# Kernel tuning notes

Hardware: AMD Instinct MI355X
Metric: run time of the kernel (lower is better)

The kernel has to match this reference:

```python
import math
import jax, jax.numpy as jnp
import numpy as np

D_MODEL = 1024
NUM_HEADS = 16
HEAD_DIM = D_MODEL // NUM_HEADS
BATCH = 4
SEQ = 2048


def setup_inputs() -> dict:
    key = jax.random.key(0)
    ks = jax.random.split(key, 9)
    scale = 1.0 / math.sqrt(D_MODEL)
    return {
        "x": jax.random.normal(ks[0], (BATCH, SEQ, D_MODEL), dtype=jnp.float32),
        "wq": jax.random.normal(ks[1], (D_MODEL, D_MODEL), dtype=jnp.float32) * scale,
        "bq": jnp.zeros((D_MODEL,), dtype=jnp.float32),
        "wk": jax.random.normal(ks[2], (D_MODEL, D_MODEL), dtype=jnp.float32) * scale,
        "bk": jnp.zeros((D_MODEL,), dtype=jnp.float32),
        "wv": jax.random.normal(ks[3], (D_MODEL, D_MODEL), dtype=jnp.float32) * scale,
        "bv": jnp.zeros((D_MODEL,), dtype=jnp.float32),
        "wo": jax.random.normal(ks[4], (D_MODEL, D_MODEL), dtype=jnp.float32) * scale,
        "bo": jnp.zeros((D_MODEL,), dtype=jnp.float32),
    }


def _split_heads(t):
    b, s, _ = t.shape
    return t.reshape(b, s, NUM_HEADS, HEAD_DIM).transpose(0, 2, 1, 3)  # [b,h,s,d]


def reference(x, wq, bq, wk, bk, wv, bv, wo, bo):
    # Linear layers: y = x @ W^T + b (torch nn.Linear convention)
    q = _split_heads(x @ wq.T + bq)
    k = _split_heads(x @ wk.T + bk)
    v = _split_heads(x @ wv.T + bv)
    scores = jnp.einsum("bhqd,bhkd->bhqk", q, k) / math.sqrt(HEAD_DIM)
    attn_weights = jax.nn.softmax(scores, axis=-1)  # dropout=0.0 (eval) -> identity
    context = jnp.einsum("bhqk,bhkd->bhqd", attn_weights, v)
    context = context.transpose(0, 2, 1, 3).reshape(x.shape[0], x.shape[1], D_MODEL)
    output = context @ wo.T + bo
    return output, attn_weights
```

## Files before the change

kernel.cpp:

```cpp
#include <hip/hip_runtime.h>
#include <cstdint>
#include <cstddef>


#define D_MODEL 1024
#define NHEADS  16
#define HDIM    64
#define BATCH   4
#define SEQ     2048
#define NTOK    (BATCH*SEQ)

typedef __bf16 bf16x8 __attribute__((ext_vector_type(8)));
typedef float  f32x4  __attribute__((ext_vector_type(4)));
typedef unsigned short u16x8 __attribute__((ext_vector_type(8)));

__device__ __forceinline__ uint16_t f2bf(float f) {
  union { float f; uint32_t u; } v; v.f = f;
  return (uint16_t)((v.u + 0x7FFFu + ((v.u >> 16) & 1u)) >> 16);
}
__device__ __forceinline__ float bf2f(uint16_t u) {
  union { uint32_t u; float f; } v; v.u = (uint32_t)u << 16; return v.f;
}
__device__ __forceinline__ bf16x8 ldbf8(const uint16_t* p) {
  return __builtin_bit_cast(bf16x8, *(const u16x8*)p);
}
__device__ __forceinline__ void nt_store4(float* p, float a, float b, float c, float d) {
  f32x4 v = { a, b, c, d };
  __builtin_nontemporal_store(v, (f32x4*)p);
}
#define MFMA16(a, b, c) __builtin_amdgcn_mfma_f32_16x16x32_bf16((a), (b), (c), 0, 0, 0)

__device__ __forceinline__ void gl_lds16(const uint16_t* g, uint16_t* l) {
  __builtin_amdgcn_global_load_lds(
      (const __attribute__((address_space(1))) uint32_t*)g,
      (__attribute__((address_space(3))) uint32_t*)l, 16, 0, 0);
}

__global__ __launch_bounds__(256) void cvt_kernel(const float* __restrict__ src,
                                                  uint16_t* __restrict__ dst, int n4) {
  int i = blockIdx.x * blockDim.x + threadIdx.x;
  if (i < n4) {
    float4 f = ((const float4*)src)[i];
    ushort4 o;
    o.x = f2bf(f.x); o.y = f2bf(f.y); o.z = f2bf(f.z); o.w = f2bf(f.w);
    ((ushort4*)dst)[i] = o;
  }
}
__global__ __launch_bounds__(256)
void cvt_w_kernel(const float* __restrict__ wq, const float* __restrict__ wk,
                  const float* __restrict__ wv, const float* __restrict__ wo,
                  uint16_t* __restrict__ dst) {
  int i = blockIdx.x * blockDim.x + threadIdx.x;
  int sel = i >> 18, off = i & 262143;
  const float* src = (sel == 0) ? wq : (sel == 1) ? wk : (sel == 2) ? wv : wo;
  float4 f = ((const float4*)src)[off];
  ushort4 o;
  o.x = f2bf(f.x); o.y = f2bf(f.y); o.z = f2bf(f.z); o.w = f2bf(f.w);
  ((ushort4*)dst)[i] = o;
}

__global__ __launch_bounds__(256)
void gemm_qkv(const uint16_t* __restrict__ A, const uint16_t* __restrict__ Wqkv,
              const float* __restrict__ bq, const float* __restrict__ bk,
              const float* __restrict__ bv,
              uint16_t* __restrict__ Qb, uint16_t* __restrict__ Kc,
              uint16_t* __restrict__ Vt) {
  __shared__ uint16_t As[128 * 64];
  __shared__ uint16_t Bs[128 * 64];
  const int flat = blockIdx.x;
  const int l = (flat & 7) * 192 + (flat >> 3);
  const int bx = l % 24, by = l / 24;
  const int tid  = threadIdx.x;
  const int lane = tid & 63;
  const int wave = tid >> 6;
  const int wr = wave >> 1, wc = wave & 1;
  const int m0 = by * 128, n0 = bx * 128;
  const int lrow = lane & 15;
  const int grp  = lane >> 4;
  const int l8   = lane >> 3;
  const int c8   = lane & 7;

  f32x4 acc[4][4] = {};

  for (int k0 = 0; k0 < 1024; k0 += 64) {
#pragma unroll
    for (int it = 0; it < 4; ++it) {
      const int chunk = wave * 4 + it;
      const int row = chunk * 8 + l8;
      gl_lds16(&A   [(size_t)(m0 + row) * 1024 + k0 + c8 * 8], &As[chunk * 512]);
      gl_lds16(&Wqkv[(size_t)(n0 + row) * 1024 + k0 + c8 * 8], &Bs[chunk * 512]);
    }
    __syncthreads();
#pragma unroll
    for (int ks = 0; ks < 2; ++ks) {
      bf16x8 af[4], bfr[4];
#pragma unroll
      for (int i = 0; i < 4; ++i) {
        af [i] = ldbf8(&As[(wr * 64 + i * 16 + lrow) * 64 + ks * 32 + grp * 8]);
        bfr[i] = ldbf8(&Bs[(wc * 64 + i * 16 + lrow) * 64 + ks * 32 + grp * 8]);
      }
#pragma unroll
      for (int i = 0; i < 4; ++i)
#pragma unroll
        for (int j = 0; j < 4; ++j)
          acc[i][j] = MFMA16(af[i], bfr[j], acc[i][j]);
    }
    __syncthreads();
  }

  const int seg = n0 >> 10;
  const float* bp = (seg == 0) ? bq : (seg == 1) ? bk : bv;
  uint16_t* dst01 = (seg == 0) ? Qb : Kc;
  const int r0 = grp * 4;
#pragma unroll
  for (int i = 0; i < 4; ++i) {
#pragma unroll
    for (int j = 0; j < 4; ++j) {
      int gmb = m0 + wr * 64 + i * 16 + r0;
      int gn  = n0 + wc * 64 + j * 16 + lrow;
      int nloc = gn & 1023;
      float bv_ = bp[nloc];
      if (seg < 2) {
#pragma unroll
        for (int r = 0; r < 4; ++r)
          dst01[(size_t)(gmb + r) * 1024 + nloc] = f2bf(acc[i][j][r] + bv_);
      } else {
        int b = gmb >> 11, s = gmb & (SEQ - 1);
        int h = nloc >> 6, d = nloc & (HDIM - 1);
        ushort4 w;
        w.x = f2bf(acc[i][j][0] + bv_);
        w.y = f2bf(acc[i][j][1] + bv_);
        w.z = f2bf(acc[i][j][2] + bv_);
        w.w = f2bf(acc[i][j][3] + bv_);
        *(ushort4*)&Vt[(((size_t)(b * NHEADS + h) * HDIM + d) << 11) + s] = w;
      }
    }
  }
}

__global__ __launch_bounds__(256)
void gemm_out(const uint16_t* __restrict__ A, const uint16_t* __restrict__ Bt,
              const float* __restrict__ bias, float* __restrict__ out) {
  __shared__ uint16_t As[128 * 64];
  __shared__ uint16_t Bs[128 * 64];
  const int flat = blockIdx.x;
  const int l = (flat & 7) * 64 + (flat >> 3);
  const int bx = l & 7, by = l >> 3;
  const int tid  = threadIdx.x;
  const int lane = tid & 63;
  const int wave = tid >> 6;
  const int wr = wave >> 1, wc = wave & 1;
  const int m0 = by * 128, n0 = bx * 128;
  const int lrow = lane & 15;
  const int grp  = lane >> 4;
  const int l8   = lane >> 3;
  const int c8   = lane & 7;

  f32x4 acc[4][4] = {};

  for (int k0 = 0; k0 < 1024; k0 += 64) {
#pragma unroll
    for (int it = 0; it < 4; ++it) {
      const int chunk = wave * 4 + it;
      const int row = chunk * 8 + l8;
      gl_lds16(&A [(size_t)(m0 + row) * 1024 + k0 + c8 * 8], &As[chunk * 512]);
      gl_lds16(&Bt[(size_t)(n0 + row) * 1024 + k0 + c8 * 8], &Bs[chunk * 512]);
    }
    __syncthreads();
#pragma unroll
    for (int ks = 0; ks < 2; ++ks) {
      bf16x8 af[4], bfr[4];
#pragma unroll
      for (int i = 0; i < 4; ++i) {
        af [i] = ldbf8(&As[(wr * 64 + i * 16 + lrow) * 64 + ks * 32 + grp * 8]);
        bfr[i] = ldbf8(&Bs[(wc * 64 + i * 16 + lrow) * 64 + ks * 32 + grp * 8]);
      }
#pragma unroll
      for (int i = 0; i < 4; ++i)
#pragma unroll
        for (int j = 0; j < 4; ++j)
          acc[i][j] = MFMA16(af[i], bfr[j], acc[i][j]);
    }
    __syncthreads();
  }

  const int r0 = grp * 4;
#pragma unroll
  for (int i = 0; i < 4; ++i) {
#pragma unroll
    for (int j = 0; j < 4; ++j) {
      int gmb = m0 + wr * 64 + i * 16 + r0;
      int gn  = n0 + wc * 64 + j * 16 + lrow;
      float bv = bias[gn];
#pragma unroll
      for (int r = 0; r < 4; ++r)
        __builtin_nontemporal_store(acc[i][j][r] + bv,
                                    &out[(size_t)(gmb + r) * 1024 + gn]);
    }
  }
}

__device__ __forceinline__ bf16x8 rd_tile(const uint16_t* t, int r, int s) {
  return ldbf8(&t[r * 64 + ((s ^ (r & 7)) * 8)]);
}

#define QBLK 128
__global__ __launch_bounds__(512)
void attn_kernel(const uint16_t* __restrict__ Q, const uint16_t* __restrict__ Kb,
                 const uint16_t* __restrict__ Vt, float* __restrict__ attnw,
                 uint16_t* __restrict__ ctx) {
  __shared__ uint16_t Ks[2][64 * 64];
  __shared__ uint16_t Vs[2][64 * 64];
  __shared__ uint16_t Pl[8][16 * 72];
  const int tid  = threadIdx.x;
  const int lane = tid & 63;
  const int wave = tid >> 6;
  const int flat = blockIdx.x;
  const int lb = (flat & 7) * 128 + (flat >> 3);
  const int qt = lb & 15, h = (lb >> 4) & 15, b = lb >> 8;
  const int q0 = qt * QBLK + wave * 16;
  const int lrow = lane & 15;
  const int grp  = lane >> 4;
  const float c = 0.125f * 1.44269504088896f;

  const uint16_t* Kh = Kb + (size_t)(b * SEQ) * D_MODEL + h * HDIM;
  const uint16_t* Vh = Vt + ((size_t)(b * NHEADS + h) * HDIM) * SEQ;

  const size_t qbase = ((size_t)(b * SEQ) + q0 + lrow) * D_MODEL + h * HDIM;
  const bf16x8 qf0 = ldbf8(&Q[qbase + grp * 8]);
  const bf16x8 qf1 = ldbf8(&Q[qbase + 32 + grp * 8]);

  const int srow = wave * 8 + (lane >> 3);
  const int scb  = (lane & 7) ^ (srow & 7);

  float l = 0.f;
  gl_lds16(&Kh[(size_t)srow * D_MODEL + scb * 8], &Ks[0][wave * 512]);
#pragma unroll 1
  for (int kc = 0; kc < SEQ / 64; ++kc) {
    const int cur = kc & 1;
    __syncthreads();
    if (kc + 1 < SEQ / 64)
      gl_lds16(&Kh[(size_t)((kc + 1) * 64 + srow) * D_MODEL + scb * 8],
               &Ks[cur ^ 1][wave * 512]);
    const uint16_t* kt_ = Ks[cur];
    f32x4 s[4];
    __builtin_amdgcn_s_setprio(1);
#pragma unroll
    for (int kt = 0; kt < 4; ++kt) {
      f32x4 a = {};
      a = MFMA16(rd_tile(kt_, kt * 16 + lrow, grp),     qf0, a);
      a = MFMA16(rd_tile(kt_, kt * 16 + lrow, 4 + grp), qf1, a);
      s[kt] = a;
    }
    __builtin_amdgcn_s_setprio(0);
    float sum = 0.f;
#pragma unroll
    for (int kt = 0; kt < 4; ++kt)
#pragma unroll
      for (int r = 0; r < 4; ++r)
        sum += __builtin_amdgcn_exp2f(s[kt][r] * c);
    l += sum;
  }
  l += __shfl_xor(l, 16);
  l += __shfl_xor(l, 32);
  const float rinv = 1.0f / l;

  f32x4 cacc[4] = {};
  uint16_t* pw = &Pl[wave][0];
  float* awc = attnw + (((size_t)(b * NHEADS + h)) * SEQ + q0) * SEQ;
  gl_lds16(&Kh[(size_t)srow * D_MODEL + scb * 8], &Ks[0][wave * 512]);
  gl_lds16(&Vh[(size_t)srow * SEQ + scb * 8],     &Vs[0][wave * 512]);
#pragma unroll 1
  for (int kc = 0; kc < SEQ / 64; ++kc) {
    const int cur = kc & 1;
    __syncthreads();
    if (kc + 1 < SEQ / 64) {
      gl_lds16(&Kh[(size_t)((kc + 1) * 64 + srow) * D_MODEL + scb * 8],
               &Ks[cur ^ 1][wave * 512]);
      gl_lds16(&Vh[(size_t)srow * SEQ + (kc + 1) * 64 + scb * 8],
               &Vs[cur ^ 1][wave * 512]);
    }
    const uint16_t* kt_ = Ks[cur];
    f32x4 s[4];
    __builtin_amdgcn_s_setprio(1);
#pragma unroll
    for (int kt = 0; kt < 4; ++kt) {
      f32x4 a = {};
      a = MFMA16(rd_tile(kt_, kt * 16 + lrow, grp),     qf0, a);
      a = MFMA16(rd_tile(kt_, kt * 16 + lrow, 4 + grp), qf1, a);
      s[kt] = a;
    }
    __builtin_amdgcn_s_setprio(0);
#pragma unroll
    for (int kt = 0; kt < 4; ++kt) {
      ushort4 w;
      w.x = f2bf(__builtin_amdgcn_exp2f(s[kt][0] * c) * rinv);
      w.y = f2bf(__builtin_amdgcn_exp2f(s[kt][1] * c) * rinv);
      w.z = f2bf(__builtin_amdgcn_exp2f(s[kt][2] * c) * rinv);
      w.w = f2bf(__builtin_amdgcn_exp2f(s[kt][3] * c) * rinv);
      *(ushort4*)&pw[lrow * 72 + kt * 16 + grp * 4] = w;
    }
    asm volatile("s_waitcnt lgkmcnt(0)" ::: "memory");
#pragma unroll
    for (int ii = 0; ii < 4; ++ii) {
      int q = ii * 4 + grp;
      ushort4 t4 = *(const ushort4*)&pw[q * 72 + lrow * 4];
      nt_store4(&awc[(size_t)q * SEQ + kc * 64 + lrow * 4],
                bf2f(t4.x), bf2f(t4.y), bf2f(t4.z), bf2f(t4.w));
    }
    const uint16_t* vt_ = Vs[cur];
    __builtin_amdgcn_s_setprio(1);
#pragma unroll
    for (int ks = 0; ks < 2; ++ks) {
      const bf16x8 pf = ldbf8(&pw[lrow * 72 + ks * 32 + grp * 8]);
#pragma unroll
      for (int n = 0; n < 4; ++n) {
        const bf16x8 vf = rd_tile(vt_, n * 16 + lrow, ks * 4 + grp);
        cacc[n] = MFMA16(pf, vf, cacc[n]);
      }
    }
    __builtin_amdgcn_s_setprio(0);
  }
#pragma unroll
  for (int n = 0; n < 4; ++n)
#pragma unroll
    for (int r = 0; r < 4; ++r) {
      int gq = q0 + grp * 4 + r;
      ctx[((size_t)(b * SEQ) + gq) * D_MODEL + h * HDIM + n * 16 + lrow] = f2bf(cacc[n][r]);
    }
}

extern "C" void kernel_launch(void* const* d_in, const int* in_sizes, int n_in,
                              void* d_out, int out_size, void* d_ws, size_t ws_size,
                              hipStream_t stream) {
  const float* x  = (const float*)d_in[0];
  const float* wq = (const float*)d_in[1];
  const float* bq = (const float*)d_in[2];
  const float* wk = (const float*)d_in[3];
  const float* bk = (const float*)d_in[4];
  const float* wv = (const float*)d_in[5];
  const float* bv = (const float*)d_in[6];
  const float* wo = (const float*)d_in[7];
  const float* bo = (const float*)d_in[8];

  char* ws = (char*)d_ws;
  uint16_t* xb   = (uint16_t*)ws;
  uint16_t* wqkv = (uint16_t*)(ws + (16u << 20));
  uint16_t* wob  = (uint16_t*)(ws + (22u << 20));
  uint16_t* Qb   = (uint16_t*)(ws + (24u << 20));
  uint16_t* Kc   = (uint16_t*)(ws + (40u << 20));
  uint16_t* Vtb  = (uint16_t*)(ws + (56u << 20));
  uint16_t* ctx  = xb;

  float* outp  = (float*)d_out;
  float* attnw = outp + (size_t)NTOK * D_MODEL;

  {
    int n4 = (NTOK * D_MODEL) / 4;
    cvt_kernel<<<(n4 + 255) / 256, 256, 0, stream>>>(x, xb, n4);
    cvt_w_kernel<<<(4 * 262144) / 256, 256, 0, stream>>>(wq, wk, wv, wo, wqkv);
  }

  gemm_qkv<<<1536, 256, 0, stream>>>(xb, wqkv, bq, bk, bv, Qb, Kc, Vtb);

  attn_kernel<<<1024, 512, 0, stream>>>(Qb, Kc, Vtb, attnw, ctx);

  gemm_out<<<512, 256, 0, stream>>>(ctx, wob, bo, outp);
}
```

Baseline: 367.1 us.

## Enlarge QKV GEMM tiles to 256x256 with double-buffered swizzled LDS

The QKV projection GEMM moves from 128x128 tiles with 4 waves to 256x256 tiles with 8 waves, each wave computing a 128x64 sub-tile. Global-to-LDS loads are double-buffered with explicit vmcnt waits so the next K-tile loads while the current one computes. The LDS layout is XOR-swizzled to avoid bank conflicts. The grid shrinks from 1536 to 384 blocks, which cuts global traffic per FLOP but uses 128KB of LDS and many more accumulator registers, so occupancy drops and wave-quantization over the CUs worsens.

```diff
diff --git a/kernel.cpp b/kernel.cpp
--- a/kernel.cpp
+++ b/kernel.cpp
@@ -34,6 +34,10 @@
   __builtin_amdgcn_global_load_lds(
       (const __attribute__((address_space(1))) uint32_t*)g,
       (__attribute__((address_space(3))) uint32_t*)l, 16, 0, 0);
+}
+
+__device__ __forceinline__ bf16x8 rd_tile(const uint16_t* t, int r, int s) {
+  return ldbf8(&t[r * 64 + ((s ^ (r & 7)) * 8)]);
 }
 
 __global__ __launch_bounds__(256) void cvt_kernel(const float* __restrict__ src,
@@ -59,53 +63,76 @@
   ((ushort4*)dst)[i] = o;
 }
 
-__global__ __launch_bounds__(256)
+__global__ __launch_bounds__(512)
 void gemm_qkv(const uint16_t* __restrict__ A, const uint16_t* __restrict__ Wqkv,
               const float* __restrict__ bq, const float* __restrict__ bk,
               const float* __restrict__ bv,
               uint16_t* __restrict__ Qb, uint16_t* __restrict__ Kc,
               uint16_t* __restrict__ Vt) {
-  __shared__ uint16_t As[128 * 64];
-  __shared__ uint16_t Bs[128 * 64];
-  const int flat = blockIdx.x;
-  const int l = (flat & 7) * 192 + (flat >> 3);
-  const int bx = l % 24, by = l / 24;
+  __shared__ uint16_t Abuf[2][256 * 64];
+  __shared__ uint16_t Bbuf[2][256 * 64];
   const int tid  = threadIdx.x;
   const int lane = tid & 63;
   const int wave = tid >> 6;
-  const int wr = wave >> 1, wc = wave & 1;
-  const int m0 = by * 128, n0 = bx * 128;
+  const int wm = wave >> 2, wn = wave & 3;
+  const int flat = blockIdx.x;
+  const int l = (flat & 7) * 48 + (flat >> 3);
+  const int bx = l % 12, by = l / 12;
+  const int m0 = by * 256, n0 = bx * 256;
   const int lrow = lane & 15;
   const int grp  = lane >> 4;
-  const int l8   = lane >> 3;
-  const int c8   = lane & 7;
-
-  f32x4 acc[4][4] = {};
-
-  for (int k0 = 0; k0 < 1024; k0 += 64) {
-#pragma unroll
-    for (int it = 0; it < 4; ++it) {
-      const int chunk = wave * 4 + it;
-      const int row = chunk * 8 + l8;
-      gl_lds16(&A   [(size_t)(m0 + row) * 1024 + k0 + c8 * 8], &As[chunk * 512]);
-      gl_lds16(&Wqkv[(size_t)(n0 + row) * 1024 + k0 + c8 * 8], &Bs[chunk * 512]);
-    }
-    __syncthreads();
+  const int sr8  = lane >> 3;
+  const int sc   = lane & 7;
+
+  f32x4 acc[8][4] = {};
+
+  auto stageTile = [&](int t, int buf) {
+    const int kof = t * 64;
+#pragma unroll
+    for (int h = 0; h < 2; ++h)
+#pragma unroll
+      for (int ch = 0; ch < 2; ++ch) {
+        const int lr  = h * 128 + wave * 16 + ch * 8 + sr8;
+        const int scb = sc ^ (lr & 7);
+        const int dof = (h * 128 + wave * 16 + ch * 8) * 64;
+        gl_lds16(&A   [(size_t)(m0 + lr) * 1024 + kof + scb * 8], &Abuf[buf][dof]);
+        gl_lds16(&Wqkv[(size_t)(n0 + lr) * 1024 + kof + scb * 8], &Bbuf[buf][dof]);
+      }
+  };
+
+  stageTile(0, 0);
+#pragma unroll 1
+  for (int t = 0; t < 16; ++t) {
+    const int c = t & 1;
+    __builtin_amdgcn_s_barrier();
+    if (t + 1 < 16) {
+      stageTile(t + 1, c ^ 1);
+      asm volatile("s_waitcnt vmcnt(8)" ::: "memory");
+    } else {
+      asm volatile("s_waitcnt vmcnt(0)" ::: "memory");
+    }
+    __builtin_amdgcn_s_barrier();
+    const uint16_t* Ab = &Abuf[c][0];
+    const uint16_t* Bb = &Bbuf[c][0];
 #pragma unroll
     for (int ks = 0; ks < 2; ++ks) {
-      bf16x8 af[4], bfr[4];
-#pragma unroll
-      for (int i = 0; i < 4; ++i) {
-        af [i] = ldbf8(&As[(wr * 64 + i * 16 + lrow) * 64 + ks * 32 + grp * 8]);
-        bfr[i] = ldbf8(&Bs[(wc * 64 + i * 16 + lrow) * 64 + ks * 32 + grp * 8]);
-      }
-#pragma unroll
-      for (int i = 0; i < 4; ++i)
-#pragma unroll
-        for (int j = 0; j < 4; ++j)
-          acc[i][j] = MFMA16(af[i], bfr[j], acc[i][j]);
-    }
-    __syncthreads();
+      bf16x8 bfr[4];
+#pragma unroll
+      for (int j = 0; j < 4; ++j)
+        bfr[j] = rd_tile(Bb, wn * 64 + j * 16 + lrow, ks * 4 + grp);
+#pragma unroll
+      for (int half = 0; half < 2; ++half) {
+        bf16x8 af[4];
+#pragma unroll
+        for (int i = 0; i < 4; ++i)
+          af[i] = rd_tile(Ab, wm * 128 + half * 64 + i * 16 + lrow, ks * 4 + grp);
+#pragma unroll
+        for (int i = 0; i < 4; ++i)
+#pragma unroll
+          for (int j = 0; j < 4; ++j)
+            acc[half * 4 + i][j] = MFMA16(af[i], bfr[j], acc[half * 4 + i][j]);
+      }
+    }
   }
 
   const int seg = n0 >> 10;
@@ -113,25 +140,25 @@
   uint16_t* dst01 = (seg == 0) ? Qb : Kc;
   const int r0 = grp * 4;
 #pragma unroll
-  for (int i = 0; i < 4; ++i) {
+  for (int I = 0; I < 8; ++I) {
 #pragma unroll
     for (int j = 0; j < 4; ++j) {
-      int gmb = m0 + wr * 64 + i * 16 + r0;
-      int gn  = n0 + wc * 64 + j * 16 + lrow;
+      int gmb = m0 + wm * 128 + I * 16 + r0;
+      int gn  = n0 + wn * 64 + j * 16 + lrow;
       int nloc = gn & 1023;
       float bv_ = bp[nloc];
       if (seg < 2) {
 #pragma unroll
         for (int r = 0; r < 4; ++r)
-          dst01[(size_t)(gmb + r) * 1024 + nloc] = f2bf(acc[i][j][r] + bv_);
+          dst01[(size_t)(gmb + r) * 1024 + nloc] = f2bf(acc[I][j][r] + bv_);
       } else {
         int b = gmb >> 11, s = gmb & (SEQ - 1);
         int h = nloc >> 6, d = nloc & (HDIM - 1);
         ushort4 w;
-        w.x = f2bf(acc[i][j][0] + bv_);
-        w.y = f2bf(acc[i][j][1] + bv_);
-        w.z = f2bf(acc[i][j][2] + bv_);
-        w.w = f2bf(acc[i][j][3] + bv_);
+        w.x = f2bf(acc[I][j][0] + bv_);
+        w.y = f2bf(acc[I][j][1] + bv_);
+        w.z = f2bf(acc[I][j][2] + bv_);
+        w.w = f2bf(acc[I][j][3] + bv_);
         *(ushort4*)&Vt[(((size_t)(b * NHEADS + h) * HDIM + d) << 11) + s] = w;
       }
     }
@@ -198,10 +225,6 @@
                                     &out[(size_t)(gmb + r) * 1024 + gn]);
     }
   }
-}
-
-__device__ __forceinline__ bf16x8 rd_tile(const uint16_t* t, int r, int s) {
-  return ldbf8(&t[r * 64 + ((s ^ (r & 7)) * 8)]);
 }
 
 #define QBLK 128
@@ -361,7 +384,7 @@
     cvt_w_kernel<<<(4 * 262144) / 256, 256, 0, stream>>>(wq, wk, wv, wo, wqkv);
   }
 
-  gemm_qkv<<<1536, 256, 0, stream>>>(xb, wqkv, bq, bk, bv, Qb, Kc, Vtb);
+  gemm_qkv<<<384, 512, 0, stream>>>(xb, wqkv, bq, bk, bv, Qb, Kc, Vtb);
 
   attn_kernel<<<1024, 512, 0, stream>>>(Qb, Kc, Vtb, attnw, ctx);
 
```

Result: faster. 356.0 us, median of 2 (-3.0%).
